# Kernel tuning notes

Measured on AMD Instinct MI355X. Metric: run time of the kernel, lower is better.

## Reference

```python
import jax, jax.numpy as jnp
import numpy as np

N_USERS = 100000
N_MOVIES = 100000
E = 1000000
D = 64
R = 5


def setup_inputs() -> dict:
    key = jax.random.key(0)
    k1, k2, k3, k4, k5 = jax.random.split(key, 5)
    z_user = jax.random.normal(k1, (N_USERS, D), dtype=jnp.float32)
    z_movie = jax.random.normal(k2, (N_MOVIES, D), dtype=jnp.float32)
    row = jax.random.randint(k3, (E,), 0, N_USERS)
    col = jax.random.randint(k4, (E,), 0, N_MOVIES)
    edge_label_index = jnp.stack([row, col], axis=0).astype(jnp.int64)
    Q = jax.random.normal(k5, (R, D, D), dtype=jnp.float32)
    return {"z_user": z_user, "z_movie": z_movie,
            "edge_label_index": edge_label_index, "Q": Q}


def reference(z_user, z_movie, edge_label_index, Q):
    row, col = edge_label_index[0], edge_label_index[1]
    u = z_user[row]        # [E, D] gathered user embeddings
    m = z_movie[col]       # [E, D] gathered movie embeddings
    # Per-edge bilinear form for each rating r: logit[e, r] = u_e^T Q_r m_e.
    # Equivalent to diag(U @ Q_r @ M^T) but O(E*D^2) instead of O(E^2*D).
    logits = jnp.einsum('ek,rkl,el->er', u, Q, m)  # [E, R]
    return jax.nn.log_softmax(logits, axis=-1)
```

## Files before the change

kernel.cpp:

```cpp
#include <hip/hip_runtime.h>
#include <stdint.h>

#define DD 64
#define RR 5

typedef float f32x4 __attribute__((ext_vector_type(4)));
typedef short short8 __attribute__((ext_vector_type(8)));
typedef __bf16 bf16x8 __attribute__((ext_vector_type(8)));

union BF8 { bf16x8 h; short8 s; };

__device__ __forceinline__ short8 pack_bf16(f32x4 a, f32x4 b) {
    BF8 u;
#pragma unroll
    for (int j = 0; j < 4; ++j) { u.h[j] = (__bf16)a[j]; u.h[4 + j] = (__bf16)b[j]; }
    return u.s;
}

struct Rows {
    f32x4 m0, m1, m2, m3;
    f32x4 u0, u1, u2, u3;
};

__launch_bounds__(256, 2)
__global__ void bilinear_decoder_kernel(
    const float* __restrict__ z_user,
    const float* __restrict__ z_movie,
    const int*   __restrict__ eidx,
    const float* __restrict__ Qm,
    float*       __restrict__ out,
    int E)
{
    const int lane = threadIdx.x & 63;
    const int wid  = threadIdx.x >> 6;
    const int q    = lane >> 4;
    const int lm   = lane & 15;

    __shared__ float st_lds[4][80];

    short8 Aq[RR][4][2];
#pragma unroll
    for (int r = 0; r < RR; ++r)
#pragma unroll
        for (int kt = 0; kt < 4; ++kt)
#pragma unroll
            for (int s = 0; s < 2; ++s) {
                const float* src = Qm + (((size_t)r * DD + kt * 16 + lm) * DD + s * 32 + q * 8);
                Aq[r][kt][s] = pack_bf16(*(const f32x4*)src, *(const f32x4*)(src + 4));
            }
#pragma unroll
    for (int r = 0; r < RR; ++r)
#pragma unroll
        for (int kt = 0; kt < 4; ++kt)
#pragma unroll
            for (int s = 0; s < 2; ++s)
                asm volatile("" : "+v"(Aq[r][kt][s]));

    const int ngroups = (E + 15) >> 4;
    const int nw = gridDim.x << 2;
    const int g0 = (blockIdx.x << 2) + wid;
    if (g0 >= ngroups) return;
    const int nsteps = (ngroups - 1 - g0) / nw + 1;

    auto ld_idx = [&](int g, int& iu, int& im) {
        int gg = g < ngroups ? g : (ngroups - 1);
        int e = (gg << 4) + lm;
        if (e >= E) e = E - 1;
        iu = eidx[e];
        im = eidx[E + e];
    };
    auto ld_rows = [&](int iu, int im, Rows& R_) {
        const float* mr = z_movie + ((size_t)im << 6);
        const float* ur = z_user  + ((size_t)iu << 6);
        R_.m0 = *(const f32x4*)(mr + q * 8);
        R_.m1 = *(const f32x4*)(mr + q * 8 + 4);
        R_.m2 = *(const f32x4*)(mr + 32 + q * 8);
        R_.m3 = *(const f32x4*)(mr + 32 + q * 8 + 4);
        R_.u0 = *(const f32x4*)(ur + q * 4);
        R_.u1 = *(const f32x4*)(ur + 16 + q * 4);
        R_.u2 = *(const f32x4*)(ur + 32 + q * 4);
        R_.u3 = *(const f32x4*)(ur + 48 + q * 4);
    };
    auto compute = [&](const Rows& R_, int g, bool store) {
        const short8 Bm0 = pack_bf16(R_.m0, R_.m1);
        const short8 Bm1 = pack_bf16(R_.m2, R_.m3);
        float lg[RR];
#pragma unroll
        for (int r = 0; r < RR; ++r) {
            float p = 0.f;
#pragma unroll
            for (int kt = 0; kt < 4; ++kt) {
                f32x4 c = {0.f, 0.f, 0.f, 0.f};
                c = __builtin_amdgcn_mfma_f32_16x16x32_bf16(Aq[r][kt][0], Bm0, c, 0, 0, 0);
                c = __builtin_amdgcn_mfma_f32_16x16x32_bf16(Aq[r][kt][1], Bm1, c, 0, 0, 0);
                const f32x4 uf = (kt == 0) ? R_.u0 : (kt == 1) ? R_.u1 : (kt == 2) ? R_.u2 : R_.u3;
#pragma unroll
                for (int rg = 0; rg < 4; ++rg)
                    p = fmaf(uf[rg], c[rg], p);
            }
            p += __shfl_xor(p, 16);
            p += __shfl_xor(p, 32);
            lg[r] = p;
        }
        float mx = lg[0];
#pragma unroll
        for (int r = 1; r < RR; ++r) mx = fmaxf(mx, lg[r]);
        float sum = 0.f;
#pragma unroll
        for (int r = 0; r < RR; ++r) sum += __expf(lg[r] - mx);
        const float sub = mx + __logf(sum);

        const float v0 = (q == 0) ? lg[0] : (q == 1) ? lg[1] : (q == 2) ? lg[2] : lg[3];
        st_lds[wid][lm * 5 + q] = v0 - sub;
        if (q == 0) st_lds[wid][lm * 5 + 4] = lg[4] - sub;

        if (store) {
            const size_t o = (size_t)g * (16 * RR);
            const size_t lim = (size_t)E * RR;
            if (o + lane < lim)              out[o + lane]      = st_lds[wid][lane];
            if (lane < 16 && o + 64 + lane < lim) out[o + 64 + lane] = st_lds[wid][64 + lane];
        }
    };

    int iuA, imA, iuB, imB;
    Rows RA, RB;
    int gA = g0;
    int gB = g0 + nw;
    ld_idx(gA, iuA, imA);
    ld_rows(iuA, imA, RA);
    ld_idx(gB, iuB, imB);

    for (int i = 0; i < nsteps; i += 2) {
        ld_rows(iuB, imB, RB);
        ld_idx(gA + 2 * nw, iuA, imA);
        compute(RA, gA, true);

        ld_rows(iuA, imA, RA);
        ld_idx(gB + 2 * nw, iuB, imB);
        compute(RB, gB, (i + 1) < nsteps);

        gA += 2 * nw;
        gB += 2 * nw;
    }
}

extern "C" void kernel_launch(void* const* d_in, const int* in_sizes, int n_in,
                              void* d_out, int out_size, void* d_ws, size_t ws_size,
                              hipStream_t stream) {
    const float* z_user  = (const float*)d_in[0];
    const float* z_movie = (const float*)d_in[1];
    const int*   eidx    = (const int*)d_in[2];
    const float* Qm      = (const float*)d_in[3];
    float* out = (float*)d_out;

    const int E = in_sizes[2] / 2;
    const int ngroups = (E + 15) >> 4;
    int nblocks = (ngroups + 3) / 4;
    if (nblocks > 512) nblocks = 512;

    bilinear_decoder_kernel<<<nblocks, 256, 0, stream>>>(
        z_user, z_movie, eidx, Qm, out, E);
}
```

Baseline: 179.2 us.

## Pre-convert embedding tables to bf16 and gather half-width rows per edge

Adds a pre-pass that converts both embedding tables to bf16 in the workspace each call. The main kernel then gathers bf16 rows, halving random-gather bytes, and keeps Q fragments in LDS instead of registers. Each wave now handles 32 edges per step, and occupancy rises to 3 blocks per CU. The trade-off is that the conversion pass must read all 51 MB of fp32 tables and write 25.6 MB every call, while the edge gather touches only part of them. The user vector also loses precision because it is now stored in bf16.

```diff
diff --git a/kernel.cpp b/kernel.cpp
--- a/kernel.cpp
+++ b/kernel.cpp
@@ -3,11 +3,13 @@
 
 #define DD 64
 #define RR 5
-
-typedef float f32x4 __attribute__((ext_vector_type(4)));
-typedef short short8 __attribute__((ext_vector_type(8)));
-typedef __bf16 bf16x8 __attribute__((ext_vector_type(8)));
-
+#define NWAVES 4
+#define BLOCK 256
+
+typedef float  f32x4   __attribute__((ext_vector_type(4)));
+typedef short  short4b __attribute__((ext_vector_type(4)));
+typedef short  short8  __attribute__((ext_vector_type(8)));
+typedef __bf16 bf16x8  __attribute__((ext_vector_type(8)));
 union BF8 { bf16x8 h; short8 s; };
 
 __device__ __forceinline__ short8 pack_bf16(f32x4 a, f32x4 b) {
@@ -16,26 +18,160 @@
     for (int j = 0; j < 4; ++j) { u.h[j] = (__bf16)a[j]; u.h[4 + j] = (__bf16)b[j]; }
     return u.s;
 }
-
-struct Rows {
-    f32x4 m0, m1, m2, m3;
-    f32x4 u0, u1, u2, u3;
-};
-
-__launch_bounds__(256, 2)
-__global__ void bilinear_decoder_kernel(
-    const float* __restrict__ z_user,
-    const float* __restrict__ z_movie,
+__device__ __forceinline__ float bf2f(short h) {
+    union { uint32_t u; float f; } v; v.u = ((uint32_t)(unsigned short)h) << 16;
+    return v.f;
+}
+
+__global__ void cvt_bf16_kernel(const float* __restrict__ a, int n8a,
+                                const float* __restrict__ b, int n8b,
+                                unsigned short* __restrict__ oa,
+                                unsigned short* __restrict__ ob) {
+    int i = blockIdx.x * blockDim.x + threadIdx.x;
+    const int stride = gridDim.x * blockDim.x;
+    const int tot = n8a + n8b;
+    for (; i < tot; i += stride) {
+        const float* src; unsigned short* dst; int j;
+        if (i < n8a) { src = a; dst = oa; j = i; }
+        else         { src = b; dst = ob; j = i - n8a; }
+        const float* p = src + (size_t)j * 8;
+        *(short8*)(dst + (size_t)j * 8) = pack_bf16(*(const f32x4*)p, *(const f32x4*)(p + 4));
+    }
+}
+
+__launch_bounds__(BLOCK, 3)
+__global__ void bilinear_bf16_kernel(
+    const unsigned short* __restrict__ zu,
+    const unsigned short* __restrict__ zm,
     const int*   __restrict__ eidx,
     const float* __restrict__ Qm,
     float*       __restrict__ out,
     int E)
 {
+    __shared__ short8 qf[RR * 8][64];
+    __shared__ float  st[NWAVES][160];
+
+    const int tid  = threadIdx.x;
+    const int wid  = tid >> 6;
+    const int lane = tid & 63;
+    const int q    = lane >> 4;
+    const int lm   = lane & 15;
+
+#pragma unroll
+    for (int t = 0; t < 10; ++t) {
+        const int f = wid * 10 + t;
+        const int r = f >> 3, kt = (f >> 1) & 3, s = f & 1;
+        const float* src = Qm + (((size_t)r * DD + kt * 16 + lm) * DD + s * 32 + q * 8);
+        qf[f][lane] = pack_bf16(*(const f32x4*)src, *(const f32x4*)(src + 4));
+    }
+    __syncthreads();
+
+    const int ng = (E + 31) >> 5;
+    const int NW = (int)gridDim.x * NWAVES;
+    int g = (int)blockIdx.x * NWAVES + wid;
+    if (g >= ng) return;
+
+    struct Half { short8 bm0, bm1; short4b u0, u1, u2, u3; };
+
+    auto ldidx = [&](int gg, int h, int& a, int& b) {
+        int e = (((gg < ng) ? gg : ng - 1) << 5) + h * 16 + lm;
+        if (e >= E) e = E - 1;
+        a = eidx[e];
+        b = eidx[E + e];
+    };
+    auto ldrows = [&](int iu, int im, Half& H) {
+        const unsigned short* mr = zm + ((size_t)im << 6);
+        const unsigned short* ur = zu + ((size_t)iu << 6);
+        H.bm0 = *(const short8*)(mr + q * 8);
+        H.bm1 = *(const short8*)(mr + 32 + q * 8);
+        H.u0  = *(const short4b*)(ur + q * 4);
+        H.u1  = *(const short4b*)(ur + 16 + q * 4);
+        H.u2  = *(const short4b*)(ur + 32 + q * 4);
+        H.u3  = *(const short4b*)(ur + 48 + q * 4);
+    };
+    auto finish = [&](const float lg[RR], int h) {
+        float mx = fmaxf(fmaxf(fmaxf(lg[0], lg[1]), fmaxf(lg[2], lg[3])), lg[4]);
+        float ssum = 0.f;
+#pragma unroll
+        for (int r = 0; r < RR; ++r) ssum += __expf(lg[r] - mx);
+        const float sub = mx + __logf(ssum);
+        const int b = h * 80 + lm * 5;
+        const float v0 = (q == 0) ? lg[0] : (q == 1) ? lg[1] : (q == 2) ? lg[2] : lg[3];
+        st[wid][b + q] = v0 - sub;
+        if (q == 0) st[wid][b + 4] = lg[4] - sub;
+    };
+    auto compute2 = [&](const Half& H0, const Half& H1, int gg) {
+        float lg0[RR], lg1[RR];
+#pragma unroll
+        for (int r = 0; r < RR; ++r) {
+            float p0 = 0.f, p1 = 0.f;
+#pragma unroll
+            for (int kt = 0; kt < 4; ++kt) {
+                const short8 a0 = qf[r * 8 + kt * 2 + 0][lane];
+                const short8 a1 = qf[r * 8 + kt * 2 + 1][lane];
+                f32x4 c0 = {0.f, 0.f, 0.f, 0.f}, c1 = {0.f, 0.f, 0.f, 0.f};
+                c0 = __builtin_amdgcn_mfma_f32_16x16x32_bf16(a0, H0.bm0, c0, 0, 0, 0);
+                c0 = __builtin_amdgcn_mfma_f32_16x16x32_bf16(a1, H0.bm1, c0, 0, 0, 0);
+                c1 = __builtin_amdgcn_mfma_f32_16x16x32_bf16(a0, H1.bm0, c1, 0, 0, 0);
+                c1 = __builtin_amdgcn_mfma_f32_16x16x32_bf16(a1, H1.bm1, c1, 0, 0, 0);
+                const short4b uc0 = (kt == 0) ? H0.u0 : (kt == 1) ? H0.u1 : (kt == 2) ? H0.u2 : H0.u3;
+                const short4b uc1 = (kt == 0) ? H1.u0 : (kt == 1) ? H1.u1 : (kt == 2) ? H1.u2 : H1.u3;
+#pragma unroll
+                for (int rg = 0; rg < 4; ++rg) {
+                    p0 = fmaf(bf2f(uc0[rg]), c0[rg], p0);
+                    p1 = fmaf(bf2f(uc1[rg]), c1[rg], p1);
+                }
+            }
+            p0 += __shfl_xor(p0, 16); p0 += __shfl_xor(p0, 32);
+            p1 += __shfl_xor(p1, 16); p1 += __shfl_xor(p1, 32);
+            lg0[r] = p0; lg1[r] = p1;
+        }
+        finish(lg0, 0);
+        finish(lg1, 1);
+        const size_t o = (size_t)gg * 160;
+        const size_t lim = (size_t)E * RR;
+        float* og = out + o;
+        if (o + lane < lim)                    og[lane]       = st[wid][lane];
+        if (o + 64 + lane < lim)               og[64 + lane]  = st[wid][64 + lane];
+        if (lane < 32 && o + 128 + lane < lim) og[128 + lane] = st[wid][128 + lane];
+    };
+
+    Half A0, A1, B0, B1;
+    int iuA0, imA0, iuA1, imA1, iuB0, imB0, iuB1, imB1;
+    int gA = g, gB = g + NW;
+    ldidx(gA, 0, iuA0, imA0); ldidx(gA, 1, iuA1, imA1);
+    ldrows(iuA0, imA0, A0);   ldrows(iuA1, imA1, A1);
+    ldidx(gB, 0, iuB0, imB0); ldidx(gB, 1, iuB1, imB1);
+    const int nsteps = (ng - 1 - g) / NW + 1;
+
+    for (int i = 0; i < nsteps; i += 2) {
+        ldrows(iuB0, imB0, B0); ldrows(iuB1, imB1, B1);
+        ldidx(gA + 2 * NW, 0, iuA0, imA0); ldidx(gA + 2 * NW, 1, iuA1, imA1);
+        compute2(A0, A1, gA);
+
+        ldrows(iuA0, imA0, A0); ldrows(iuA1, imA1, A1);
+        ldidx(gB + 2 * NW, 0, iuB0, imB0); ldidx(gB + 2 * NW, 1, iuB1, imB1);
+        if (i + 1 < nsteps) compute2(B0, B1, gB);
+
+        gA += 2 * NW;
+        gB += 2 * NW;
+    }
+}
+
+struct Rows {
+    f32x4 m0, m1, m2, m3;
+    f32x4 u0, u1, u2, u3;
+};
+__launch_bounds__(256, 2)
+__global__ void bilinear_fp32_kernel(
+    const float* __restrict__ z_user, const float* __restrict__ z_movie,
+    const int* __restrict__ eidx, const float* __restrict__ Qm,
+    float* __restrict__ out, int E)
+{
     const int lane = threadIdx.x & 63;
     const int wid  = threadIdx.x >> 6;
     const int q    = lane >> 4;
     const int lm   = lane & 15;
-
     __shared__ float st_lds[4][80];
 
     short8 Aq[RR][4][2];
@@ -48,14 +184,6 @@
                 const float* src = Qm + (((size_t)r * DD + kt * 16 + lm) * DD + s * 32 + q * 8);
                 Aq[r][kt][s] = pack_bf16(*(const f32x4*)src, *(const f32x4*)(src + 4));
             }
-#pragma unroll
-    for (int r = 0; r < RR; ++r)
-#pragma unroll
-        for (int kt = 0; kt < 4; ++kt)
-#pragma unroll
-            for (int s = 0; s < 2; ++s)
-                asm volatile("" : "+v"(Aq[r][kt][s]));
-
     const int ngroups = (E + 15) >> 4;
     const int nw = gridDim.x << 2;
     const int g0 = (blockIdx.x << 2) + wid;
@@ -66,20 +194,15 @@
         int gg = g < ngroups ? g : (ngroups - 1);
         int e = (gg << 4) + lm;
         if (e >= E) e = E - 1;
-        iu = eidx[e];
-        im = eidx[E + e];
+        iu = eidx[e]; im = eidx[E + e];
     };
     auto ld_rows = [&](int iu, int im, Rows& R_) {
         const float* mr = z_movie + ((size_t)im << 6);
         const float* ur = z_user  + ((size_t)iu << 6);
-        R_.m0 = *(const f32x4*)(mr + q * 8);
-        R_.m1 = *(const f32x4*)(mr + q * 8 + 4);
-        R_.m2 = *(const f32x4*)(mr + 32 + q * 8);
-        R_.m3 = *(const f32x4*)(mr + 32 + q * 8 + 4);
-        R_.u0 = *(const f32x4*)(ur + q * 4);
-        R_.u1 = *(const f32x4*)(ur + 16 + q * 4);
-        R_.u2 = *(const f32x4*)(ur + 32 + q * 4);
-        R_.u3 = *(const f32x4*)(ur + 48 + q * 4);
+        R_.m0 = *(const f32x4*)(mr + q * 8);      R_.m1 = *(const f32x4*)(mr + q * 8 + 4);
+        R_.m2 = *(const f32x4*)(mr + 32 + q * 8); R_.m3 = *(const f32x4*)(mr + 32 + q * 8 + 4);
+        R_.u0 = *(const f32x4*)(ur + q * 4);      R_.u1 = *(const f32x4*)(ur + 16 + q * 4);
+        R_.u2 = *(const f32x4*)(ur + 32 + q * 4); R_.u3 = *(const f32x4*)(ur + 48 + q * 4);
     };
     auto compute = [&](const Rows& R_, int g, bool store) {
         const short8 Bm0 = pack_bf16(R_.m0, R_.m1);
@@ -95,11 +218,9 @@
                 c = __builtin_amdgcn_mfma_f32_16x16x32_bf16(Aq[r][kt][1], Bm1, c, 0, 0, 0);
                 const f32x4 uf = (kt == 0) ? R_.u0 : (kt == 1) ? R_.u1 : (kt == 2) ? R_.u2 : R_.u3;
 #pragma unroll
-                for (int rg = 0; rg < 4; ++rg)
-                    p = fmaf(uf[rg], c[rg], p);
+                for (int rg = 0; rg < 4; ++rg) p = fmaf(uf[rg], c[rg], p);
             }
-            p += __shfl_xor(p, 16);
-            p += __shfl_xor(p, 32);
+            p += __shfl_xor(p, 16); p += __shfl_xor(p, 32);
             lg[r] = p;
         }
         float mx = lg[0];
@@ -109,38 +230,30 @@
 #pragma unroll
         for (int r = 0; r < RR; ++r) sum += __expf(lg[r] - mx);
         const float sub = mx + __logf(sum);
-
         const float v0 = (q == 0) ? lg[0] : (q == 1) ? lg[1] : (q == 2) ? lg[2] : lg[3];
         st_lds[wid][lm * 5 + q] = v0 - sub;
         if (q == 0) st_lds[wid][lm * 5 + 4] = lg[4] - sub;
-
         if (store) {
             const size_t o = (size_t)g * (16 * RR);
             const size_t lim = (size_t)E * RR;
-            if (o + lane < lim)              out[o + lane]      = st_lds[wid][lane];
+            if (o + lane < lim)                   out[o + lane]      = st_lds[wid][lane];
             if (lane < 16 && o + 64 + lane < lim) out[o + 64 + lane] = st_lds[wid][64 + lane];
         }
     };
-
     int iuA, imA, iuB, imB;
     Rows RA, RB;
-    int gA = g0;
-    int gB = g0 + nw;
+    int gA = g0, gB = g0 + nw;
     ld_idx(gA, iuA, imA);
     ld_rows(iuA, imA, RA);
     ld_idx(gB, iuB, imB);
-
     for (int i = 0; i < nsteps; i += 2) {
         ld_rows(iuB, imB, RB);
         ld_idx(gA + 2 * nw, iuA, imA);
         compute(RA, gA, true);
-
         ld_rows(iuA, imA, RA);
         ld_idx(gB + 2 * nw, iuB, imB);
         compute(RB, gB, (i + 1) < nsteps);
-
-        gA += 2 * nw;
-        gB += 2 * nw;
+        gA += 2 * nw; gB += 2 * nw;
     }
 }
 
@@ -154,10 +267,21 @@
     float* out = (float*)d_out;
 
     const int E = in_sizes[2] / 2;
-    const int ngroups = (E + 15) >> 4;
-    int nblocks = (ngroups + 3) / 4;
-    if (nblocks > 512) nblocks = 512;
-
-    bilinear_decoder_kernel<<<nblocks, 256, 0, stream>>>(
-        z_user, z_movie, eidx, Qm, out, E);
-}
+    const size_t need = ((size_t)in_sizes[0] + (size_t)in_sizes[1]) * sizeof(unsigned short);
+
+    if (ws_size >= need) {
+        unsigned short* zub = (unsigned short*)d_ws;
+        unsigned short* zmb = zub + in_sizes[0];
+        cvt_bf16_kernel<<<2048, 256, 0, stream>>>(z_user, in_sizes[0] / 8,
+                                                  z_movie, in_sizes[1] / 8, zub, zmb);
+        const int ng = (E + 31) >> 5;
+        int nb = (ng + NWAVES - 1) / NWAVES;
+        if (nb > 768) nb = 768;
+        bilinear_bf16_kernel<<<nb, BLOCK, 0, stream>>>(zub, zmb, eidx, Qm, out, E);
+    } else {
+        const int ngroups = (E + 15) >> 4;
+        int nblocks = (ngroups + 3) / 4;
+        if (nblocks > 512) nblocks = 512;
+        bilinear_fp32_kernel<<<nblocks, 256, 0, stream>>>(z_user, z_movie, eidx, Qm, out, E);
+    }
+}
```

New measurement: 246.2 us. 37.4% more time.
